# Kernel tuning notes

Hardware: AMD Instinct MI355X
Metric: run time of the kernel (lower is better)

The kernel has to match this reference:

```python
import jax, jax.numpy as jnp
import numpy as np

B, L, D, H = 8, 4096, 1024, 16
HD = D // H
HID = 4096  # int(D * 4.0)
KSZ = 25    # moving-average kernel size
EPS = 1e-6


def _layernorm(x, w, b):
    mu = jnp.mean(x, axis=-1, keepdims=True)
    var = jnp.mean((x - mu) ** 2, axis=-1, keepdims=True)
    return (x - mu) / jnp.sqrt(var + EPS) * w + b


def _lin(x, W, b):
    # eqx.nn.Linear stores weight as (out, in)
    return jnp.einsum('...i,oi->...o', x, W) + b


def setup_inputs() -> dict:
    key = jax.random.key(0)
    ks = jax.random.split(key, 8)
    s = 0.02
    return {
        'x': jax.random.normal(ks[0], (B, L, D), dtype=jnp.float32),
        'ln1_w': jnp.ones((D,), jnp.float32),
        'ln1_b': jnp.zeros((D,), jnp.float32),
        'Wq': jax.random.normal(ks[1], (D, D), jnp.float32) * s,
        'bq': jnp.zeros((D,), jnp.float32),
        'Wk': jax.random.normal(ks[2], (D, D), jnp.float32) * s,
        'bk': jnp.zeros((D,), jnp.float32),
        'Wv': jax.random.normal(ks[3], (D, D), jnp.float32) * s,
        'bv': jnp.zeros((D,), jnp.float32),
        'Wo': jax.random.normal(ks[4], (D, D), jnp.float32) * s,
        'bo': jnp.zeros((D,), jnp.float32),
        'ln2_w': jnp.ones((D,), jnp.float32),
        'ln2_b': jnp.zeros((D,), jnp.float32),
        'W1': jax.random.normal(ks[5], (HID, D), jnp.float32) * s,
        'b1': jnp.zeros((HID,), jnp.float32),
        'W2': jax.random.normal(ks[6], (D, HID), jnp.float32) * s,
        'b2': jnp.zeros((D,), jnp.float32),
    }


def reference(x, ln1_w, ln1_b, Wq, bq, Wk, bk, Wv, bv, Wo, bo,
              ln2_w, ln2_b, W1, b1, W2, b2):
    b, l, d = x.shape
    # --- AutoCorrelation attention on norm1(x) ---
    y = _layernorm(x, ln1_w, ln1_b)
    Q = _lin(y, Wq, bq).reshape(b, l, H, HD).transpose(0, 2, 1, 3)  # (B,H,L,hd)
    K = _lin(y, Wk, bk).reshape(b, l, H, HD).transpose(0, 2, 1, 3)
    V = _lin(y, Wv, bv).reshape(b, l, H, HD).transpose(0, 2, 1, 3)
    qf = jnp.fft.rfft(Q, axis=2)
    kf = jnp.fft.rfft(K, axis=2)
    corr_time = jnp.fft.irfft(qf * jnp.conjugate(kf), n=l, axis=2)  # (B,H,L,hd)
    corr = jnp.mean(corr_time, axis=-1)                             # (B,H,L)
    attn = jax.nn.softmax(corr, axis=-1)
    out = jnp.einsum('bhl,bhld->bhd', attn, V)                      # (B,H,hd)
    # faithful lossy reshape: transpose(0,2,1) -> (B,hd,H), flatten to (B,D)
    out = out.transpose(0, 2, 1).reshape(b, d)
    out = _lin(out, Wo, bo)
    y = jnp.broadcast_to(out[:, None, :], (b, l, d))  # repeat over L
    x = x + y
    # --- Series decomposition: depthwise moving average, subtract trend ---
    kern = jnp.ones((KSZ, 1, d), x.dtype) / KSZ
    xt = x.transpose(0, 2, 1)  # (B,D,L)
    trend = jax.lax.conv_general_dilated(
        xt, kern, window_strides=(1,), padding='SAME',
        dimension_numbers=('NCL', 'LIO', 'NCL'), feature_group_count=d)
    x = x - trend.transpose(0, 2, 1)
    # --- MLP (dropout p=0 -> identity) ---
    y = _layernorm(x, ln2_w, ln2_b)
    y = _lin(jax.nn.gelu(_lin(y, W1, b1)), W2, b2)
    return x + y
```

## Files before the change

kernel.cpp:

```cpp
#include <hip/hip_runtime.h>

#define DEV __device__ __forceinline__

typedef __attribute__((ext_vector_type(8))) short bf16x8;
typedef __attribute__((ext_vector_type(4))) float f32x4;
typedef unsigned short u16;
typedef __attribute__((address_space(1))) const void* gvp;
typedef __attribute__((address_space(3))) void* svp;

DEV u16 f2bf(float f){
  unsigned u = __float_as_uint(f);
  u = (u + 0x7FFFu + ((u >> 16) & 1u)) >> 16;
  return (u16)u;
}
DEV float bf2f(u16 v){ return __uint_as_float(((unsigned)v) << 16); }
DEV float2 cmul(float2 a, float2 b){ return make_float2(a.x*b.x - a.y*b.y, a.x*b.y + a.y*b.x); }
DEV int rev8(int i){
  return ((i & 7) << 9) | ((i & 0x38) << 3) | ((i & 0x1C0) >> 3) | ((i >> 9) & 7);
}

__global__ void k_prep(const float* __restrict__ Wq, const float* __restrict__ Wk,
                       const float* __restrict__ W1, const float* __restrict__ W2,
                       const float* __restrict__ bq, const float* __restrict__ bk,
                       u16* __restrict__ Wqkb, u16* __restrict__ W1b, u16* __restrict__ W2b,
                       float* __restrict__ bqk, float2* __restrict__ twg){
  const size_t i = (size_t)blockIdx.x * 256 + threadIdx.x;
  if (i < 1048576){
    Wqkb[i] = f2bf(Wq[i]);
  } else if (i < 2097152){
    Wqkb[i] = f2bf(Wk[i - 1048576]);
  } else if (i < 6291456){
    W1b[i - 2097152] = f2bf(W1[i - 2097152]);
  } else if (i < 10485760){
    W2b[i - 6291456] = f2bf(W2[i - 6291456]);
  } else if (i < 10487808){
    const int k = (int)(i - 10485760);
    float sn, cs;
    sincosf(-1.5339807878856412e-03f * (float)k, &sn, &cs);
    twg[k] = make_float2(cs, sn);
  } else if (i < 10488832){
    const int k = (int)(i - 10487808);
    bqk[k] = bq[k]; bqk[1024 + k] = bk[k];
  }
}

__global__ __launch_bounds__(256) void k_ln(const float* __restrict__ x, const float* __restrict__ w,
                                            const float* __restrict__ b, u16* __restrict__ y){
  const int row = blockIdx.x;
  const int tid = threadIdx.x;
  const float4 v = ((const float4*)(x + (size_t)row * 1024))[tid];
  float s1 = v.x + v.y + v.z + v.w;
  float s2 = v.x*v.x + v.y*v.y + v.z*v.z + v.w*v.w;
  #pragma unroll
  for (int o = 32; o > 0; o >>= 1){ s1 += __shfl_down(s1, o); s2 += __shfl_down(s2, o); }
  __shared__ float r1[4], r2[4];
  __shared__ float mu_s, rs_s;
  const int wv = tid >> 6;
  if ((tid & 63) == 0){ r1[wv] = s1; r2[wv] = s2; }
  __syncthreads();
  if (tid == 0){
    float t1 = r1[0]+r1[1]+r1[2]+r1[3], t2 = r2[0]+r2[1]+r2[2]+r2[3];
    float mu = t1 * (1.0f/1024.0f);
    float var = t2 * (1.0f/1024.0f) - mu*mu;
    mu_s = mu; rs_s = rsqrtf(var + 1e-6f);
  }
  __syncthreads();
  const float mu = mu_s, rs = rs_s;
  const float4 wv4 = ((const float4*)w)[tid];
  const float4 bv4 = ((const float4*)b)[tid];
  ushort4 o4;
  o4.x = f2bf((v.x-mu)*rs*wv4.x + bv4.x);
  o4.y = f2bf((v.y-mu)*rs*wv4.y + bv4.y);
  o4.z = f2bf((v.z-mu)*rs*wv4.z + bv4.z);
  o4.w = f2bf((v.w-mu)*rs*wv4.w + bv4.w);
  ((ushort4*)(y + (size_t)row*1024))[tid] = o4;
}

template<int MODE>
__launch_bounds__(512, 2)
__global__ void k_gemm5(const u16* __restrict__ A, const u16* __restrict__ Bw,
                        const float* __restrict__ bias, void* __restrict__ out, void* __restrict__ out2,
                        int M, int N, int K)
{
  __shared__ __align__(16) u16 SMEM[65536];
  u16 (*LA)[16384] = reinterpret_cast<u16(*)[16384]>(SMEM);
  u16 (*LB)[16384] = reinterpret_cast<u16(*)[16384]>(SMEM + 32768);
  const int tid = threadIdx.x;
  const int wave = tid >> 6, lane = tid & 63;
  const int l15 = lane & 15, l4 = lane >> 4;
  const int wrq = wave >> 2, wcq = wave & 3;
  (void)M;

  const int nwg = gridDim.x;
  const int q8 = nwg >> 3;
  const int wg = (blockIdx.x & 7) * q8 + (blockIdx.x >> 3);
  const int NBN = N >> 8;
  const int bm = wg / NBN, bn = wg % NBN;
  const int NT = K >> 6, NI = NT >> 1;

  const int sr8 = lane >> 3;
  const int sch8 = ((lane & 7) ^ (sr8 & 7)) * 8;
  const u16* gA = A  + ((size_t)(bm*256 + wave*16 + sr8)) * K + sch8;
  const u16* gB = Bw + ((size_t)(bn*256 + wave*16 + sr8)) * K + sch8;
  const size_t gH = (size_t)128 * K;
  const size_t gJ = (size_t)8 * K;
  const int lbase = wave * 1024;

  const unsigned swzb = (unsigned)((l4 ^ (l15 & 7)) * 16);
  const unsigned uA0  = (unsigned)(uintptr_t)&LA[0][0] + (unsigned)((wrq*64 + l15)*128) + swzb;
  const unsigned uB0  = (unsigned)(uintptr_t)&LB[0][0] + (unsigned)((wcq*32 + l15)*128) + swzb;
  const unsigned uA0x = uA0 ^ 64u, uB0x = uB0 ^ 64u;
  const unsigned uA1  = uA0 + 32768u, uA1x = uA0x + 32768u;
  const unsigned uB1  = uB0 + 32768u, uB1x = uB0x + 32768u;

  f32x4 acc[8][4];
  const f32x4 z4 = {0.f, 0.f, 0.f, 0.f};
  #pragma unroll
  for (int m = 0; m < 8; ++m)
    #pragma unroll
    for (int n = 0; n < 4; ++n) acc[m][n] = z4;

#define DSR(dst, base, OFF) asm volatile("ds_read_b128 %0, %1 offset:" #OFF : "=v"(dst) : "v"(base))

#define LDA_Q0(b0, b1) do{ \
  DSR(fa[0], b0, 0);    DSR(fa[1], b1, 0); \
  DSR(fa[2], b0, 2048); DSR(fa[3], b1, 2048); \
  DSR(fa[4], b0, 4096); DSR(fa[5], b1, 4096); \
  DSR(fa[6], b0, 6144); DSR(fa[7], b1, 6144); }while(0)
#define LDA_Q1(b0, b1) do{ \
  DSR(fa[0], b0, 16384); DSR(fa[1], b1, 16384); \
  DSR(fa[2], b0, 18432); DSR(fa[3], b1, 18432); \
  DSR(fa[4], b0, 20480); DSR(fa[5], b1, 20480); \
  DSR(fa[6], b0, 22528); DSR(fa[7], b1, 22528); }while(0)
#define LDB_Q0(dst, b0, b1) do{ \
  DSR(dst[0], b0, 0);    DSR(dst[1], b1, 0); \
  DSR(dst[2], b0, 2048); DSR(dst[3], b1, 2048); }while(0)
#define LDB_Q1(dst, b0, b1) do{ \
  DSR(dst[0], b0, 16384); DSR(dst[1], b1, 16384); \
  DSR(dst[2], b0, 18432); DSR(dst[3], b1, 18432); }while(0)

#define STG(LD, G, DB, HALF, TK) do{ \
    const int tk_ = (TK) < NT ? (TK) : NT - 1; \
    const u16* g_ = (G) + (size_t)tk_ * 64 + (size_t)(HALF) * gH; \
    u16* l_ = &LD[DB][lbase + (HALF) * 8192]; \
    __builtin_amdgcn_global_load_lds((gvp)g_,        (svp)l_,        16, 0, 0); \
    __builtin_amdgcn_global_load_lds((gvp)(g_ + gJ), (svp)(l_ + 512),16, 0, 0); \
  }while(0)

#define MFMA16(QA, QB, FB) do{ \
    __builtin_amdgcn_s_setprio(1); \
    _Pragma("unroll") for (int kk = 0; kk < 2; ++kk) \
    _Pragma("unroll") for (int mm = 0; mm < 4; ++mm) \
    _Pragma("unroll") for (int nn = 0; nn < 2; ++nn) \
      acc[(QA)*4+mm][(QB)*2+nn] = __builtin_amdgcn_mfma_f32_16x16x32_bf16( \
          fa[mm*2+kk], FB[nn*2+kk], acc[(QA)*4+mm][(QB)*2+nn], 0, 0, 0); \
    __builtin_amdgcn_s_setprio(0); \
  }while(0)

#define SBAR  __builtin_amdgcn_s_barrier()
#define SB0   __builtin_amdgcn_sched_barrier(0)
#define LGKM0 do{ asm volatile("s_waitcnt lgkmcnt(0)" ::: "memory"); SB0; }while(0)
#define LGKM8 asm volatile("s_waitcnt lgkmcnt(8)" ::: "memory")
#define VM4   asm volatile("s_waitcnt vmcnt(4)" ::: "memory")

  STG(LA, gA, 0, 0, 0); STG(LA, gA, 0, 1, 0);
  STG(LB, gB, 0, 0, 0); STG(LB, gB, 0, 1, 0);
  STG(LA, gA, 1, 0, 1);
  STG(LB, gB, 1, 1, 1);
  VM4; SBAR;

  for (int it = 0; it < NI; ++it){
    const int u = 2 * it;
    bf16x8 fa[8], fbA[4], fbB[4];
    LDB_Q0(fbA, uB0, uB0x);
    LDA_Q0(uA0, uA0x);
    STG(LA, gA, 1, 1, u+1); STG(LB, gB, 1, 0, u+1);
    LGKM8;
    SBAR; LGKM0; MFMA16(0, 0, fbA); SB0; SBAR;
    LDB_Q1(fbB, uB0, uB0x);
    SBAR; LGKM0; MFMA16(0, 1, fbB); SB0; SBAR;
    LDA_Q1(uA0, uA0x);
    STG(LA, gA, 0, 0, u+2);
    SBAR; LGKM0; MFMA16(1, 1, fbB); SB0; SBAR;
    STG(LB, gB, 0, 1, u+2);
    VM4; SBAR; SB0; MFMA16(1, 0, fbA); SB0; SBAR;
    LDB_Q0(fbA, uB1, uB1x);
    LDA_Q0(uA1, uA1x);
    STG(LA, gA, 0, 1, u+2); STG(LB, gB, 0, 0, u+2);
    LGKM8;
    SBAR; LGKM0; MFMA16(0, 0, fbA); SB0; SBAR;
    LDB_Q1(fbB, uB1, uB1x);
    SBAR; LGKM0; MFMA16(0, 1, fbB); SB0; SBAR;
    LDA_Q1(uA1, uA1x);
    STG(LA, gA, 1, 0, u+3);
    SBAR; LGKM0; MFMA16(1, 1, fbB); SB0; SBAR;
    STG(LB, gB, 1, 1, u+3);
    VM4; SBAR; SB0; MFMA16(1, 0, fbA); SB0; SBAR;
  }
#undef DSR
#undef LDA_Q0
#undef LDA_Q1
#undef LDB_Q0
#undef LDB_Q1
#undef STG
#undef MFMA16
#undef SBAR
#undef SB0
#undef LGKM0
#undef LGKM8
#undef VM4

  if (MODE == 3){
    asm volatile("s_waitcnt vmcnt(0)" ::: "memory");
    __syncthreads();
    u16* T = SMEM;
    const int bq = bm >> 4;
    const int l0 = (bm & 15) * 256;
    u16* dstb = (u16*)(bn < 4 ? out : out2) + ((size_t)bq*1024 + (bn & 3)*256)*4096 + l0;
    #pragma unroll
    for (int half = 0; half < 2; ++half){
      #pragma unroll
      for (int nn = 0; nn < 2; ++nn){
        const int n = half*2 + nn;
        const int colh = wcq*32 + nn*16 + l15;
        const float bv = bias[bn*256 + half*128 + colh];
        #pragma unroll
        for (int m = 0; m < 8; ++m){
          const int lrow = (m>>2)*128 + wrq*64 + (m&3)*16 + l4*4;
          ushort4 o4;
          o4.x = f2bf(acc[m][n][0] + bv);
          o4.y = f2bf(acc[m][n][1] + bv);
          o4.z = f2bf(acc[m][n][2] + bv);
          o4.w = f2bf(acc[m][n][3] + bv);
          *(ushort4*)&T[colh*264 + lrow] = o4;
        }
      }
      __syncthreads();
      {
        const int c = tid >> 2, lch = (tid & 3) * 64;
        u16* drow = dstb + (size_t)(half*128 + c) * 4096 + lch;
        const u16* srow = &T[c*264 + lch];
        #pragma unroll
        for (int i = 0; i < 8; ++i)
          *(bf16x8*)(drow + i*8) = *(const bf16x8*)(srow + i*8);
      }
      __syncthreads();
    }
  } else {
    #pragma unroll
    for (int m = 0; m < 8; ++m){
      const int gr0 = bm*256 + (m>>2)*128 + wrq*64 + (m&3)*16 + l4*4;
      #pragma unroll
      for (int n = 0; n < 4; ++n){
        const int gc = bn*256 + (n>>1)*128 + wcq*32 + (n&1)*16 + l15;
        const float bv = bias[gc];
        #pragma unroll
        for (int r2 = 0; r2 < 4; ++r2){
          const size_t off = (size_t)(gr0 + r2) * N + gc;
          float v = acc[m][n][r2] + bv;
          if (MODE == 1){
            const float a = 0.7978845608028654f * (v + 0.044715f * v * v * v);
            const float e = __expf(2.0f * a);
            const float th = (e - 1.0f) / (e + 1.0f);
            ((u16*)out)[off] = f2bf(0.5f * v * (1.0f + th));
          } else {
            float* op = (float*)out;
            op[off] += v;
          }
        }
      }
    }
  }
}

DEV void fft4096_dif8(float2* Z, const float2* __restrict__ tw, int tid){
  const float C = 0.70710678118654752f;
  #pragma unroll
  for (int s = 4; s >= 1; --s){
    const int q = 1 << (3*(s-1));
    const int step = 1 << (12 - 3*s);
    #pragma unroll
    for (int tt = tid; tt < 512; tt += 256){
      const int j = tt & (q-1);
      const int base = ((tt >> (3*(s-1))) << (3*s)) + j;
      float2 a0 = Z[base],       a1 = Z[base+q],   a2 = Z[base+2*q], a3 = Z[base+3*q];
      float2 a4 = Z[base+4*q],   a5 = Z[base+5*q], a6 = Z[base+6*q], a7 = Z[base+7*q];
      float2 e0 = {a0.x+a4.x, a0.y+a4.y}, o0 = {a0.x-a4.x, a0.y-a4.y};
      float2 e1 = {a2.x+a6.x, a2.y+a6.y}, o1 = {a2.x-a6.x, a2.y-a6.y};
      float2 e2 = {a1.x+a5.x, a1.y+a5.y}, o2 = {a1.x-a5.x, a1.y-a5.y};
      float2 e3 = {a3.x+a7.x, a3.y+a7.y}, o3 = {a3.x-a7.x, a3.y-a7.y};
      float2 E0 = {e0.x+e1.x, e0.y+e1.y}, E1 = {e0.x-e1.x, e0.y-e1.y};
      float2 E2 = {e2.x+e3.x, e2.y+e3.y}, E3 = {e2.x-e3.x, e2.y-e3.y};
      float2 u0 = {E0.x+E2.x, E0.y+E2.y};
      float2 u4 = {E0.x-E2.x, E0.y-E2.y};
      float2 njE3 = {E3.y, -E3.x};
      float2 u2 = {E1.x+njE3.x, E1.y+njE3.y};
      float2 u6 = {E1.x-njE3.x, E1.y-njE3.y};
      float2 W1o2 = {C*(o2.x+o2.y), C*(o2.y-o2.x)};
      float2 W3o2 = {C*(o2.y-o2.x), -C*(o2.x+o2.y)};
      float2 W1o3 = {C*(o3.x+o3.y), C*(o3.y-o3.x)};
      float2 W3o3 = {C*(o3.y-o3.x), -C*(o3.x+o3.y)};
      float2 njo1 = {o1.y, -o1.x};
      float2 u1 = {o0.x + W1o2.x + njo1.x + W3o3.x, o0.y + W1o2.y + njo1.y + W3o3.y};
      float2 u3 = {o0.x + W3o2.x - njo1.x + W1o3.x, o0.y + W3o2.y - njo1.y + W1o3.y};
      float2 u5 = {o0.x - W1o2.x + njo1.x - W3o3.x, o0.y - W1o2.y + njo1.y - W3o3.y};
      float2 u7 = {o0.x - W3o2.x - njo1.x - W1o3.x, o0.y - W3o2.y - njo1.y - W1o3.y};
      const float2 w1 = tw[j*step];
      const float2 w2 = tw[2*j*step];
      const float2 w4 = tw[4*j*step];
      const float2 w3 = cmul(w1, w2);
      const float2 w5 = cmul(w1, w4);
      const float2 w6 = cmul(w2, w4);
      const float2 w7 = cmul(w3, w4);
      Z[base]     = u0;
      Z[base+q]   = cmul(u1, w1);
      Z[base+2*q] = cmul(u2, w2);
      Z[base+3*q] = cmul(u3, w3);
      Z[base+4*q] = cmul(u4, w4);
      Z[base+5*q] = cmul(u5, w5);
      Z[base+6*q] = cmul(u6, w6);
      Z[base+7*q] = cmul(u7, w7);
    }
    __syncthreads();
  }
}

DEV void fft4096_dit8_inv(float2* Z, const float2* __restrict__ tw, int tid){
  const float C = 0.70710678118654752f;
  #pragma unroll
  for (int s = 1; s <= 4; ++s){
    const int q = 1 << (3*(s-1));
    const int step = 1 << (12 - 3*s);
    #pragma unroll
    for (int tt = tid; tt < 512; tt += 256){
      const int j = tt & (q-1);
      const int base = ((tt >> (3*(s-1))) << (3*s)) + j;
      float2 a0 = Z[base],       a1 = Z[base+q],   a2 = Z[base+2*q], a3 = Z[base+3*q];
      float2 a4 = Z[base+4*q],   a5 = Z[base+5*q], a6 = Z[base+6*q], a7 = Z[base+7*q];
      float2 w1 = tw[j*step];   w1.y = -w1.y;
      float2 w2 = tw[2*j*step]; w2.y = -w2.y;
      float2 w4 = tw[4*j*step]; w4.y = -w4.y;
      const float2 w3 = cmul(w1, w2);
      const float2 w5 = cmul(w1, w4);
      const float2 w6 = cmul(w2, w4);
      const float2 w7 = cmul(w3, w4);
      a1 = cmul(a1, w1); a2 = cmul(a2, w2); a3 = cmul(a3, w3);
      a4 = cmul(a4, w4); a5 = cmul(a5, w5); a6 = cmul(a6, w6); a7 = cmul(a7, w7);
      float2 e0 = {a0.x+a4.x, a0.y+a4.y}, o0 = {a0.x-a4.x, a0.y-a4.y};
      float2 e1 = {a2.x+a6.x, a2.y+a6.y}, o1 = {a2.x-a6.x, a2.y-a6.y};
      float2 e2 = {a1.x+a5.x, a1.y+a5.y}, o2 = {a1.x-a5.x, a1.y-a5.y};
      float2 e3 = {a3.x+a7.x, a3.y+a7.y}, o3 = {a3.x-a7.x, a3.y-a7.y};
      float2 E0 = {e0.x+e1.x, e0.y+e1.y}, E1 = {e0.x-e1.x, e0.y-e1.y};
      float2 E2 = {e2.x+e3.x, e2.y+e3.y}, E3 = {e2.x-e3.x, e2.y-e3.y};
      float2 pjE3 = {-E3.y, E3.x};
      float2 W1o2 = {C*(o2.x-o2.y), C*(o2.x+o2.y)};
      float2 W3o2 = {-C*(o2.x+o2.y), C*(o2.x-o2.y)};
      float2 W1o3 = {C*(o3.x-o3.y), C*(o3.x+o3.y)};
      float2 W3o3 = {-C*(o3.x+o3.y), C*(o3.x-o3.y)};
      float2 pjo1 = {-o1.y, o1.x};
      Z[base]     = make_float2(E0.x+E2.x, E0.y+E2.y);
      Z[base+q]   = make_float2(o0.x + W1o2.x + pjo1.x + W3o3.x, o0.y + W1o2.y + pjo1.y + W3o3.y);
      Z[base+2*q] = make_float2(E1.x+pjE3.x, E1.y+pjE3.y);
      Z[base+3*q] = make_float2(o0.x + W3o2.x - pjo1.x + W1o3.x, o0.y + W3o2.y - pjo1.y + W1o3.y);
      Z[base+4*q] = make_float2(E0.x-E2.x, E0.y-E2.y);
      Z[base+5*q] = make_float2(o0.x - W1o2.x + pjo1.x - W3o3.x, o0.y - W1o2.y + pjo1.y - W3o3.y);
      Z[base+6*q] = make_float2(E1.x-pjE3.x, E1.y-pjE3.y);
      Z[base+7*q] = make_float2(o0.x - W3o2.x - pjo1.x - W1o3.x, o0.y - W3o2.y - pjo1.y - W1o3.y);
    }
    __syncthreads();
  }
}

__global__ __launch_bounds__(256) void k_fftcorr(const u16* __restrict__ Qt, const u16* __restrict__ Kt,
                                                 const float2* __restrict__ twg, float* __restrict__ S){
  __shared__ float2 Z[4096];
  const int tid = threadIdx.x;
  const int bh = blockIdx.x, dg = blockIdx.y;
  float2 sa[16];
  #pragma unroll
  for (int j = 0; j < 16; ++j) sa[j] = make_float2(0.f, 0.f);
  for (int dd = 0; dd < 8; ++dd){
    const int d = dg*8 + dd;
    const u16* q  = Qt + ((size_t)bh*64 + d) * 4096;
    const u16* kp = Kt + ((size_t)bh*64 + d) * 4096;
    for (int i = tid; i < 4096; i += 256)
      Z[i] = make_float2(bf2f(q[i]), bf2f(kp[i]));
    __syncthreads();
    fft4096_dif8(Z, twg, tid);
    #pragma unroll
    for (int j = 0; j < 16; ++j){
      const int p = j*256 + tid;
      const int f = rev8(p);
      const int p2 = rev8((4096 - f) & 4095);
      const float2 a = Z[p];
      const float2 c = Z[p2];
      const float qr = 0.5f * (a.x + c.x);
      const float qi = 0.5f * (a.y - c.y);
      const float kr = 0.5f * (a.y + c.y);
      const float ki = 0.5f * (c.x - a.x);
      sa[j].x += qr*kr + qi*ki;
      sa[j].y += qi*kr - qr*ki;
    }
    __syncthreads();
  }
  float2* Sg = (float2*)S + ((size_t)dg*128 + bh) * 4096;
  #pragma unroll
  for (int j = 0; j < 16; ++j)
    Sg[j*256 + tid] = sa[j];
}

__global__ __launch_bounds__(256) void k_isoftmax(const float* __restrict__ S, const float2* __restrict__ twg,
                                                  float* __restrict__ attn){
  __shared__ float2 Z[4096];
  __shared__ float red[4];
  __shared__ float bc;
  const int tid = threadIdx.x;
  const int bh = blockIdx.x;
  const float2* S2 = (const float2*)S;
  for (int i = tid; i < 4096; i += 256){
    float2 acc = make_float2(0.f, 0.f);
    #pragma unroll
    for (int g = 0; g < 8; ++g){
      const float2 v = S2[((size_t)g*128 + bh) * 4096 + i];
      acc.x += v.x; acc.y += v.y;
    }
    Z[i] = acc;
  }
  __syncthreads();
  fft4096_dit8_inv(Z, twg, tid);
  const float scale = 1.0f / (4096.0f * 64.0f);
  float cr[16];
  float lmax = -1e30f;
  #pragma unroll
  for (int j = 0; j < 16; ++j){
    const float c = Z[j*256 + tid].x * scale;
    cr[j] = c;
    lmax = fmaxf(lmax, c);
  }
  #pragma unroll
  for (int o = 32; o > 0; o >>= 1) lmax = fmaxf(lmax, __shfl_down(lmax, o));
  if ((tid & 63) == 0) red[tid >> 6] = lmax;
  __syncthreads();
  if (tid == 0) bc = fmaxf(fmaxf(red[0], red[1]), fmaxf(red[2], red[3]));
  __syncthreads();
  const float gmax = bc;
  float lsum = 0.f;
  #pragma unroll
  for (int j = 0; j < 16; ++j){ cr[j] = __expf(cr[j] - gmax); lsum += cr[j]; }
  #pragma unroll
  for (int o = 32; o > 0; o >>= 1) lsum += __shfl_down(lsum, o);
  if ((tid & 63) == 0) red[tid >> 6] = lsum;
  __syncthreads();
  if (tid == 0) bc = red[0] + red[1] + red[2] + red[3];
  __syncthreads();
  const float inv = 1.0f / bc;
  float* at = attn + (size_t)bh * 4096;
  #pragma unroll
  for (int j = 0; j < 16; ++j) at[j*256 + tid] = cr[j] * inv;
}

__global__ __launch_bounds__(256) void k_yw(const float* __restrict__ attn, const u16* __restrict__ Y,
                                            float* __restrict__ yw){
  __shared__ float at[128*20 + 4];
  const int b = blockIdx.x, lq = blockIdx.y;
  const int l0 = lq * 128;
  const int tid = threadIdx.x;
  for (int idx = tid; idx < 2048; idx += 256){
    const int h = idx >> 7, l = idx & 127;
    at[l*20 + h] = attn[((size_t)b*16 + h)*4096 + l0 + l];
  }
  __syncthreads();
  float acc[16][4];
  #pragma unroll
  for (int h = 0; h < 16; ++h)
    #pragma unroll
    for (int j = 0; j < 4; ++j) acc[h][j] = 0.f;
  const u16* yb = Y + ((size_t)b*4096 + l0)*1024 + tid*4;
  for (int l = 0; l < 128; ++l){
    const ushort4 yv4 = *(const ushort4*)(yb + (size_t)l*1024);
    const float y0 = bf2f(yv4.x), y1 = bf2f(yv4.y), y2 = bf2f(yv4.z), y3 = bf2f(yv4.w);
    #pragma unroll
    for (int hq = 0; hq < 4; ++hq){
      const float4 a4 = *(const float4*)&at[l*20 + hq*4];
      acc[hq*4+0][0] += a4.x*y0; acc[hq*4+0][1] += a4.x*y1; acc[hq*4+0][2] += a4.x*y2; acc[hq*4+0][3] += a4.x*y3;
      acc[hq*4+1][0] += a4.y*y0; acc[hq*4+1][1] += a4.y*y1; acc[hq*4+1][2] += a4.y*y2; acc[hq*4+1][3] += a4.y*y3;
      acc[hq*4+2][0] += a4.z*y0; acc[hq*4+2][1] += a4.z*y1; acc[hq*4+2][2] += a4.z*y2; acc[hq*4+2][3] += a4.z*y3;
      acc[hq*4+3][0] += a4.w*y0; acc[hq*4+3][1] += a4.w*y1; acc[hq*4+3][2] += a4.w*y2; acc[hq*4+3][3] += a4.w*y3;
    }
  }
  float* ywb = yw + (size_t)b*16*1024 + tid*4;
  #pragma unroll
  for (int h = 0; h < 16; ++h)
    #pragma unroll
    for (int j = 0; j < 4; ++j)
      atomicAdd(&ywb[(size_t)h*1024 + j], acc[h][j]);
}

__global__ __launch_bounds__(256) void k_vproj(const float* __restrict__ yw, const float* __restrict__ Wv,
                                               const float* __restrict__ bv, float* __restrict__ oav){
  __shared__ float yv[1024];
  const int b = blockIdx.x, h = blockIdx.y;
  const int tid = threadIdx.x;
  for (int i = tid; i < 1024; i += 256) yv[i] = yw[((size_t)b*16 + h)*1024 + i];
  __syncthreads();
  const int hd = tid >> 2, q = tid & 3;
  const float4* wr = (const float4*)(Wv + (size_t)(h*64 + hd)*1024 + q*256);
  float acc = 0.f;
  #pragma unroll 4
  for (int i = 0; i < 64; ++i){
    const float4 w4 = wr[i];
    acc += yv[q*256+4*i]*w4.x + yv[q*256+4*i+1]*w4.y + yv[q*256+4*i+2]*w4.z + yv[q*256+4*i+3]*w4.w;
  }
  acc += __shfl_xor(acc, 1);
  acc += __shfl_xor(acc, 2);
  if (q == 0) oav[(size_t)b*1024 + hd*16 + h] = acc + bv[h*64 + hd];
}

__global__ __launch_bounds__(256) void k_proj(const float* __restrict__ oav, const float* __restrict__ Wo,
                                              const float* __restrict__ bo, float* __restrict__ proj){
  const int b = blockIdx.x;
  const int o = blockIdx.y * 256 + threadIdx.x;
  __shared__ float xin[1024];
  for (int i = threadIdx.x; i < 1024; i += 256) xin[i] = oav[(size_t)b*1024 + i];
  __syncthreads();
  float acc = bo[o];
  const float4* wr = (const float4*)(Wo + (size_t)o * 1024);
  #pragma unroll 4
  for (int i = 0; i < 256; ++i){
    const float4 w4 = wr[i];
    acc += xin[4*i]*w4.x + xin[4*i+1]*w4.y + xin[4*i+2]*w4.z + xin[4*i+3]*w4.w;
  }
  proj[(size_t)b*1024 + o] = acc;
}

__global__ __launch_bounds__(512) void k_decln(const float* __restrict__ x, const float* __restrict__ proj,
                                               const float* __restrict__ w, const float* __restrict__ bvec,
                                               float* __restrict__ out, u16* __restrict__ y){
  __shared__ float red1[8], red2[8];
  __shared__ float mu_s, rs_s;
  const int b = blockIdx.x, lc = blockIdx.y;
  const int tid = threadIdx.x;
  const int l0 = lc * 64;
  const float* xb = x + (size_t)b*4096*1024;
  float* ob = out + (size_t)b*4096*1024;
  u16* yb = y + (size_t)b*4096*1024;
  float pv[2], wv[2], bv[2], wsum[2];
  #pragma unroll
  for (int j = 0; j < 2; ++j){
    const int d = tid + j*512;
    pv[j] = proj[(size_t)b*1024 + d];
    wv[j] = w[d]; bv[j] = bvec[d];
    wsum[j] = 0.f;
  }
  float cnt = 0.f;
  const int lo = (l0 - 12 < 0) ? 0 : l0 - 12;
  for (int ll = lo; ll <= l0 + 11; ++ll){
    #pragma unroll
    for (int j = 0; j < 2; ++j) wsum[j] += xb[(size_t)ll*1024 + tid + j*512];
    cnt += 1.f;
  }
  for (int l = l0; l < l0 + 64; ++l){
    if (l + 12 < 4096){
      #pragma unroll
      for (int j = 0; j < 2; ++j) wsum[j] += xb[(size_t)(l+12)*1024 + tid + j*512];
      cnt += 1.f;
    }
    float x2[2];
    float s1 = 0.f, s2 = 0.f;
    #pragma unroll
    for (int j = 0; j < 2; ++j){
      const float xc = xb[(size_t)l*1024 + tid + j*512];
      x2[j] = xc + pv[j] - (wsum[j] + cnt*pv[j]) * 0.04f;
      ob[(size_t)l*1024 + tid + j*512] = x2[j];
      s1 += x2[j]; s2 += x2[j]*x2[j];
    }
    #pragma unroll
    for (int o = 32; o > 0; o >>= 1){ s1 += __shfl_down(s1, o); s2 += __shfl_down(s2, o); }
    if ((tid & 63) == 0){ red1[tid >> 6] = s1; red2[tid >> 6] = s2; }
    __syncthreads();
    if (tid == 0){
      float t1 = 0.f, t2 = 0.f;
      #pragma unroll
      for (int k = 0; k < 8; ++k){ t1 += red1[k]; t2 += red2[k]; }
      const float mu = t1 * (1.0f/1024.0f);
      mu_s = mu; rs_s = rsqrtf(t2*(1.0f/1024.0f) - mu*mu + 1e-6f);
    }
    __syncthreads();
    const float mu = mu_s, rs = rs_s;
    #pragma unroll
    for (int j = 0; j < 2; ++j)
      yb[(size_t)l*1024 + tid + j*512] = f2bf((x2[j]-mu)*rs*wv[j] + bv[j]);
    if (l >= 12){
      #pragma unroll
      for (int j = 0; j < 2; ++j) wsum[j] -= xb[(size_t)(l-12)*1024 + tid + j*512];
      cnt -= 1.f;
    }
  }
}

extern "C" void kernel_launch(void* const* d_in, const int* in_sizes, int n_in,
                              void* d_out, int out_size, void* d_ws, size_t ws_size,
                              hipStream_t stream){
  const float* x    = (const float*)d_in[0];
  const float* ln1w = (const float*)d_in[1];
  const float* ln1b = (const float*)d_in[2];
  const float* Wq   = (const float*)d_in[3];
  const float* bq   = (const float*)d_in[4];
  const float* Wk   = (const float*)d_in[5];
  const float* bk   = (const float*)d_in[6];
  const float* Wv   = (const float*)d_in[7];
  const float* bv   = (const float*)d_in[8];
  const float* Wo   = (const float*)d_in[9];
  const float* bo   = (const float*)d_in[10];
  const float* ln2w = (const float*)d_in[11];
  const float* ln2b = (const float*)d_in[12];
  const float* W1   = (const float*)d_in[13];
  const float* b1   = (const float*)d_in[14];
  const float* W2   = (const float*)d_in[15];
  const float* b2   = (const float*)d_in[16];
  float* out = (float*)d_out;

  char* ws = (char*)d_ws;
  float* S  = (float*)(ws + 0);
  u16* Qt   = (u16*)(ws + 134217728);
  u16* Kt   = (u16*)(ws + 201326592);
  u16* H1   = (u16*)(ws + 0);
  u16* Y    = (u16*)(ws + 268435456);
  float2* twg = (float2*)(ws + 339738624);
  float* attn = (float*)(ws + 339755008);
  float* yw   = (float*)(ws + 341852160);
  float* oav  = (float*)(ws + 342376448);
  float* proj = (float*)(ws + 342409216);
  float* bqk  = (float*)(ws + 342441984);
  u16* Wqkb   = (u16*)(ws + 342450176);
  u16* W1b    = (u16*)(ws + 346644480);
  u16* W2b    = (u16*)(ws + 355033088);

  k_prep<<<40972, 256, 0, stream>>>(Wq, Wk, W1, W2, bq, bk, Wqkb, W1b, W2b, bqk, twg);

  k_ln<<<32768, 256, 0, stream>>>(x, ln1w, ln1b, Y);

  k_gemm5<3><<<1024, 512, 0, stream>>>(Y, Wqkb, bqk, Qt, Kt, 32768, 2048, 1024);

  k_fftcorr<<<dim3(128, 8), 256, 0, stream>>>(Qt, Kt, twg, S);
  k_isoftmax<<<128, 256, 0, stream>>>(S, twg, attn);

  hipMemsetAsync(yw, 0, 524288, stream);
  k_yw<<<dim3(8, 32), 256, 0, stream>>>(attn, Y, yw);
  k_vproj<<<dim3(8, 16), 256, 0, stream>>>(yw, Wv, bv, oav);
  k_proj<<<dim3(8, 4), 256, 0, stream>>>(oav, Wo, bo, proj);

  k_decln<<<dim3(8, 64), 512, 0, stream>>>(x, proj, ln2w, ln2b, out, Y);

  k_gemm5<1><<<2048, 512, 0, stream>>>(Y, W1b, b1, H1, nullptr, 32768, 4096, 1024);
  k_gemm5<2><<<512, 512, 0, stream>>>(H1, W2b, b2, out, nullptr, 32768, 1024, 4096);
}
```

Measured before the change: 1.260 ms.

## Fuse LN1 into prep kernel, replace yw atomics with partials, wave-per-row decomp LN

```diff
diff --git a/kernel.cpp b/kernel.cpp
--- a/kernel.cpp
+++ b/kernel.cpp
@@ -19,61 +19,62 @@
   return ((i & 7) << 9) | ((i & 0x38) << 3) | ((i & 0x1C0) >> 3) | ((i >> 9) & 7);
 }
 
-__global__ void k_prep(const float* __restrict__ Wq, const float* __restrict__ Wk,
+__global__ __launch_bounds__(256) void k_prepln(const float* __restrict__ x, const float* __restrict__ ln1w,
+                       const float* __restrict__ ln1b, u16* __restrict__ Y,
+                       const float* __restrict__ Wq, const float* __restrict__ Wk,
                        const float* __restrict__ W1, const float* __restrict__ W2,
                        const float* __restrict__ bq, const float* __restrict__ bk,
                        u16* __restrict__ Wqkb, u16* __restrict__ W1b, u16* __restrict__ W2b,
                        float* __restrict__ bqk, float2* __restrict__ twg){
-  const size_t i = (size_t)blockIdx.x * 256 + threadIdx.x;
-  if (i < 1048576){
-    Wqkb[i] = f2bf(Wq[i]);
-  } else if (i < 2097152){
-    Wqkb[i] = f2bf(Wk[i - 1048576]);
-  } else if (i < 6291456){
-    W1b[i - 2097152] = f2bf(W1[i - 2097152]);
-  } else if (i < 10485760){
-    W2b[i - 6291456] = f2bf(W2[i - 6291456]);
-  } else if (i < 10487808){
-    const int k = (int)(i - 10485760);
+  const int tid = threadIdx.x;
+  if (blockIdx.x < 32768){
+    const int row = blockIdx.x;
+    const float4 v = ((const float4*)(x + (size_t)row * 1024))[tid];
+    float s1 = v.x + v.y + v.z + v.w;
+    float s2 = v.x*v.x + v.y*v.y + v.z*v.z + v.w*v.w;
+    #pragma unroll
+    for (int o = 32; o > 0; o >>= 1){ s1 += __shfl_down(s1, o); s2 += __shfl_down(s2, o); }
+    __shared__ float r1[4], r2[4];
+    __shared__ float mu_s, rs_s;
+    const int wv = tid >> 6;
+    if ((tid & 63) == 0){ r1[wv] = s1; r2[wv] = s2; }
+    __syncthreads();
+    if (tid == 0){
+      float t1 = r1[0]+r1[1]+r1[2]+r1[3], t2 = r2[0]+r2[1]+r2[2]+r2[3];
+      float mu = t1 * (1.0f/1024.0f);
+      float var = t2 * (1.0f/1024.0f) - mu*mu;
+      mu_s = mu; rs_s = rsqrtf(var + 1e-6f);
+    }
+    __syncthreads();
+    const float mu = mu_s, rs = rs_s;
+    const float4 wv4 = ((const float4*)ln1w)[tid];
+    const float4 bv4 = ((const float4*)ln1b)[tid];
+    ushort4 o4;
+    o4.x = f2bf((v.x-mu)*rs*wv4.x + bv4.x);
+    o4.y = f2bf((v.y-mu)*rs*wv4.y + bv4.y);
+    o4.z = f2bf((v.z-mu)*rs*wv4.z + bv4.z);
+    o4.w = f2bf((v.w-mu)*rs*wv4.w + bv4.w);
+    ((ushort4*)(Y + (size_t)row*1024))[tid] = o4;
+    return;
+  }
+  const size_t j = (size_t)(blockIdx.x - 32768) * 256 + tid;
+  if (j < 1048576){
+    Wqkb[j] = f2bf(Wq[j]);
+  } else if (j < 2097152){
+    Wqkb[j] = f2bf(Wk[j - 1048576]);
+  } else if (j < 6291456){
+    W1b[j - 2097152] = f2bf(W1[j - 2097152]);
+  } else if (j < 10485760){
+    W2b[j - 6291456] = f2bf(W2[j - 6291456]);
+  } else if (j < 10487808){
+    const int k = (int)(j - 10485760);
     float sn, cs;
     sincosf(-1.5339807878856412e-03f * (float)k, &sn, &cs);
     twg[k] = make_float2(cs, sn);
-  } else if (i < 10488832){
-    const int k = (int)(i - 10487808);
+  } else if (j < 10488832){
+    const int k = (int)(j - 10487808);
     bqk[k] = bq[k]; bqk[1024 + k] = bk[k];
   }
-}
-
-__global__ __launch_bounds__(256) void k_ln(const float* __restrict__ x, const float* __restrict__ w,
-                                            const float* __restrict__ b, u16* __restrict__ y){
-  const int row = blockIdx.x;
-  const int tid = threadIdx.x;
-  const float4 v = ((const float4*)(x + (size_t)row * 1024))[tid];
-  float s1 = v.x + v.y + v.z + v.w;
-  float s2 = v.x*v.x + v.y*v.y + v.z*v.z + v.w*v.w;
-  #pragma unroll
-  for (int o = 32; o > 0; o >>= 1){ s1 += __shfl_down(s1, o); s2 += __shfl_down(s2, o); }
-  __shared__ float r1[4], r2[4];
-  __shared__ float mu_s, rs_s;
-  const int wv = tid >> 6;
-  if ((tid & 63) == 0){ r1[wv] = s1; r2[wv] = s2; }
-  __syncthreads();
-  if (tid == 0){
-    float t1 = r1[0]+r1[1]+r1[2]+r1[3], t2 = r2[0]+r2[1]+r2[2]+r2[3];
-    float mu = t1 * (1.0f/1024.0f);
-    float var = t2 * (1.0f/1024.0f) - mu*mu;
-    mu_s = mu; rs_s = rsqrtf(var + 1e-6f);
-  }
-  __syncthreads();
-  const float mu = mu_s, rs = rs_s;
-  const float4 wv4 = ((const float4*)w)[tid];
-  const float4 bv4 = ((const float4*)b)[tid];
-  ushort4 o4;
-  o4.x = f2bf((v.x-mu)*rs*wv4.x + bv4.x);
-  o4.y = f2bf((v.y-mu)*rs*wv4.y + bv4.y);
-  o4.z = f2bf((v.z-mu)*rs*wv4.z + bv4.z);
-  o4.w = f2bf((v.w-mu)*rs*wv4.w + bv4.w);
-  ((ushort4*)(y + (size_t)row*1024))[tid] = o4;
 }
 
 template<int MODE>
@@ -460,7 +461,7 @@
 }
 
 __global__ __launch_bounds__(256) void k_yw(const float* __restrict__ attn, const u16* __restrict__ Y,
-                                            float* __restrict__ yw){
+                                            float* __restrict__ yws){
   __shared__ float at[128*20 + 4];
   const int b = blockIdx.x, lq = blockIdx.y;
   const int l0 = lq * 128;
@@ -488,20 +489,26 @@
       acc[hq*4+3][0] += a4.w*y0; acc[hq*4+3][1] += a4.w*y1; acc[hq*4+3][2] += a4.w*y2; acc[hq*4+3][3] += a4.w*y3;
     }
   }
-  float* ywb = yw + (size_t)b*16*1024 + tid*4;
+  float* ywb = yws + ((size_t)(b*32 + lq)*16) * 1024 + tid*4;
   #pragma unroll
   for (int h = 0; h < 16; ++h)
     #pragma unroll
     for (int j = 0; j < 4; ++j)
-      atomicAdd(&ywb[(size_t)h*1024 + j], acc[h][j]);
-}
-
-__global__ __launch_bounds__(256) void k_vproj(const float* __restrict__ yw, const float* __restrict__ Wv,
+      ywb[(size_t)h*1024 + j] = acc[h][j];
+}
+
+__global__ __launch_bounds__(256) void k_vproj(const float* __restrict__ yws, const float* __restrict__ Wv,
                                                const float* __restrict__ bv, float* __restrict__ oav){
   __shared__ float yv[1024];
   const int b = blockIdx.x, h = blockIdx.y;
   const int tid = threadIdx.x;
-  for (int i = tid; i < 1024; i += 256) yv[i] = yw[((size_t)b*16 + h)*1024 + i];
+  for (int i = tid; i < 1024; i += 256){
+    float a = 0.f;
+    #pragma unroll 8
+    for (int g = 0; g < 32; ++g)
+      a += yws[((size_t)(b*32 + g)*16 + h)*1024 + i];
+    yv[i] = a;
+  }
   __syncthreads();
   const int hd = tid >> 2, q = tid & 3;
   const float4* wr = (const float4*)(Wv + (size_t)(h*64 + hd)*1024 + q*256);
@@ -536,63 +543,78 @@
 __global__ __launch_bounds__(512) void k_decln(const float* __restrict__ x, const float* __restrict__ proj,
                                                const float* __restrict__ w, const float* __restrict__ bvec,
                                                float* __restrict__ out, u16* __restrict__ y){
-  __shared__ float red1[8], red2[8];
-  __shared__ float mu_s, rs_s;
   const int b = blockIdx.x, lc = blockIdx.y;
-  const int tid = threadIdx.x;
-  const int l0 = lc * 64;
-  const float* xb = x + (size_t)b*4096*1024;
-  float* ob = out + (size_t)b*4096*1024;
-  u16* yb = y + (size_t)b*4096*1024;
-  float pv[2], wv[2], bv[2], wsum[2];
-  #pragma unroll
-  for (int j = 0; j < 2; ++j){
-    const int d = tid + j*512;
-    pv[j] = proj[(size_t)b*1024 + d];
-    wv[j] = w[d]; bv[j] = bvec[d];
-    wsum[j] = 0.f;
+  const int wave = threadIdx.x >> 6, lane = threadIdx.x & 63;
+  const int l0 = lc*64 + wave*8;
+  const int d0 = lane * 16;
+  const float* xb = x + (size_t)b*4096*1024 + d0;
+  float* ob = out + (size_t)b*4096*1024 + d0;
+  u16* yb = y + (size_t)b*4096*1024 + d0;
+  float pv[16], wv[16], bv[16], wsum[16];
+  #pragma unroll
+  for (int k = 0; k < 4; ++k){
+    const float4 p4 = *(const float4*)(proj + (size_t)b*1024 + d0 + k*4);
+    const float4 w4 = *(const float4*)(w + d0 + k*4);
+    const float4 b4 = *(const float4*)(bvec + d0 + k*4);
+    pv[k*4+0]=p4.x; pv[k*4+1]=p4.y; pv[k*4+2]=p4.z; pv[k*4+3]=p4.w;
+    wv[k*4+0]=w4.x; wv[k*4+1]=w4.y; wv[k*4+2]=w4.z; wv[k*4+3]=w4.w;
+    bv[k*4+0]=b4.x; bv[k*4+1]=b4.y; bv[k*4+2]=b4.z; bv[k*4+3]=b4.w;
+    wsum[k*4+0]=0.f; wsum[k*4+1]=0.f; wsum[k*4+2]=0.f; wsum[k*4+3]=0.f;
   }
   float cnt = 0.f;
   const int lo = (l0 - 12 < 0) ? 0 : l0 - 12;
-  for (int ll = lo; ll <= l0 + 11; ++ll){
-    #pragma unroll
-    for (int j = 0; j < 2; ++j) wsum[j] += xb[(size_t)ll*1024 + tid + j*512];
+  const int hi = (l0 + 11 > 4095) ? 4095 : l0 + 11;
+  for (int ll = lo; ll <= hi; ++ll){
+    #pragma unroll
+    for (int k = 0; k < 4; ++k){
+      const float4 v = *(const float4*)(xb + (size_t)ll*1024 + k*4);
+      wsum[k*4+0]+=v.x; wsum[k*4+1]+=v.y; wsum[k*4+2]+=v.z; wsum[k*4+3]+=v.w;
+    }
     cnt += 1.f;
   }
-  for (int l = l0; l < l0 + 64; ++l){
+  for (int l = l0; l < l0 + 8; ++l){
     if (l + 12 < 4096){
       #pragma unroll
-      for (int j = 0; j < 2; ++j) wsum[j] += xb[(size_t)(l+12)*1024 + tid + j*512];
+      for (int k = 0; k < 4; ++k){
+        const float4 v = *(const float4*)(xb + (size_t)(l+12)*1024 + k*4);
+        wsum[k*4+0]+=v.x; wsum[k*4+1]+=v.y; wsum[k*4+2]+=v.z; wsum[k*4+3]+=v.w;
+      }
       cnt += 1.f;
     }
-    float x2[2];
+    float x2[16];
     float s1 = 0.f, s2 = 0.f;
     #pragma unroll
-    for (int j = 0; j < 2; ++j){
-      const float xc = xb[(size_t)l*1024 + tid + j*512];
-      x2[j] = xc + pv[j] - (wsum[j] + cnt*pv[j]) * 0.04f;
-      ob[(size_t)l*1024 + tid + j*512] = x2[j];
-      s1 += x2[j]; s2 += x2[j]*x2[j];
-    }
-    #pragma unroll
-    for (int o = 32; o > 0; o >>= 1){ s1 += __shfl_down(s1, o); s2 += __shfl_down(s2, o); }
-    if ((tid & 63) == 0){ red1[tid >> 6] = s1; red2[tid >> 6] = s2; }
-    __syncthreads();
-    if (tid == 0){
-      float t1 = 0.f, t2 = 0.f;
+    for (int k = 0; k < 4; ++k){
+      const float4 v = *(const float4*)(xb + (size_t)l*1024 + k*4);
+      const float xc[4] = {v.x, v.y, v.z, v.w};
       #pragma unroll
-      for (int k = 0; k < 8; ++k){ t1 += red1[k]; t2 += red2[k]; }
-      const float mu = t1 * (1.0f/1024.0f);
-      mu_s = mu; rs_s = rsqrtf(t2*(1.0f/1024.0f) - mu*mu + 1e-6f);
-    }
-    __syncthreads();
-    const float mu = mu_s, rs = rs_s;
-    #pragma unroll
-    for (int j = 0; j < 2; ++j)
-      yb[(size_t)l*1024 + tid + j*512] = f2bf((x2[j]-mu)*rs*wv[j] + bv[j]);
+      for (int j = 0; j < 4; ++j){
+        const int idx = k*4 + j;
+        x2[idx] = xc[j] + pv[idx] - (wsum[idx] + cnt*pv[idx]) * 0.04f;
+        s1 += x2[idx]; s2 += x2[idx]*x2[idx];
+      }
+      float4 o4 = {x2[k*4+0], x2[k*4+1], x2[k*4+2], x2[k*4+3]};
+      *(float4*)(ob + (size_t)l*1024 + k*4) = o4;
+    }
+    #pragma unroll
+    for (int o = 32; o > 0; o >>= 1){ s1 += __shfl_xor(s1, o); s2 += __shfl_xor(s2, o); }
+    const float mu = s1 * (1.0f/1024.0f);
+    const float rs = rsqrtf(s2*(1.0f/1024.0f) - mu*mu + 1e-6f);
+    #pragma unroll
+    for (int k = 0; k < 4; ++k){
+      ushort4 y4;
+      y4.x = f2bf((x2[k*4+0]-mu)*rs*wv[k*4+0] + bv[k*4+0]);
+      y4.y = f2bf((x2[k*4+1]-mu)*rs*wv[k*4+1] + bv[k*4+1]);
+      y4.z = f2bf((x2[k*4+2]-mu)*rs*wv[k*4+2] + bv[k*4+2]);
+      y4.w = f2bf((x2[k*4+3]-mu)*rs*wv[k*4+3] + bv[k*4+3]);
+      *(ushort4*)(yb + (size_t)l*1024 + k*4) = y4;
+    }
     if (l >= 12){
       #pragma unroll
-      for (int j = 0; j < 2; ++j) wsum[j] -= xb[(size_t)(l-12)*1024 + tid + j*512];
+      for (int k = 0; k < 4; ++k){
+        const float4 v = *(const float4*)(xb + (size_t)(l-12)*1024 + k*4);
+        wsum[k*4+0]-=v.x; wsum[k*4+1]-=v.y; wsum[k*4+2]-=v.z; wsum[k*4+3]-=v.w;
+      }
       cnt -= 1.f;
     }
   }
@@ -621,14 +643,14 @@
   float* out = (float*)d_out;
 
   char* ws = (char*)d_ws;
-  float* S  = (float*)(ws + 0);
+  float* S    = (float*)(ws + 0);
+  float* yws  = (float*)(ws + 0);
   u16* Qt   = (u16*)(ws + 134217728);
   u16* Kt   = (u16*)(ws + 201326592);
   u16* H1   = (u16*)(ws + 0);
   u16* Y    = (u16*)(ws + 268435456);
   float2* twg = (float2*)(ws + 339738624);
   float* attn = (float*)(ws + 339755008);
-  float* yw   = (float*)(ws + 341852160);
   float* oav  = (float*)(ws + 342376448);
   float* proj = (float*)(ws + 342409216);
   float* bqk  = (float*)(ws + 342441984);
@@ -636,18 +658,16 @@
   u16* W1b    = (u16*)(ws + 346644480);
   u16* W2b    = (u16*)(ws + 355033088);
 
-  k_prep<<<40972, 256, 0, stream>>>(Wq, Wk, W1, W2, bq, bk, Wqkb, W1b, W2b, bqk, twg);
-
-  k_ln<<<32768, 256, 0, stream>>>(x, ln1w, ln1b, Y);
+  k_prepln<<<73740, 256, 0, stream>>>(x, ln1w, ln1b, Y, Wq, Wk, W1, W2, bq, bk,
+                                      Wqkb, W1b, W2b, bqk, twg);
 
   k_gemm5<3><<<1024, 512, 0, stream>>>(Y, Wqkb, bqk, Qt, Kt, 32768, 2048, 1024);
 
   k_fftcorr<<<dim3(128, 8), 256, 0, stream>>>(Qt, Kt, twg, S);
   k_isoftmax<<<128, 256, 0, stream>>>(S, twg, attn);
 
-  hipMemsetAsync(yw, 0, 524288, stream);
-  k_yw<<<dim3(8, 32), 256, 0, stream>>>(attn, Y, yw);
-  k_vproj<<<dim3(8, 16), 256, 0, stream>>>(yw, Wv, bv, oav);
+  k_yw<<<dim3(8, 32), 256, 0, stream>>>(attn, Y, yws);
+  k_vproj<<<dim3(8, 16), 256, 0, stream>>>(yws, Wv, bv, oav);
   k_proj<<<dim3(8, 4), 256, 0, stream>>>(oav, Wo, bo, proj);
 
   k_decln<<<dim3(8, 64), 512, 0, stream>>>(x, proj, ln2w, ln2b, out, Y);
```

After: 1.204 ms. 1.05x faster.
